# Kernel optimization log

Hardware: AMD Instinct MI355X
Metric: run time of the kernel (lower is better)

Reference implementation:

```python
import jax, jax.numpy as jnp
import numpy as np

FEAT_DOWNSAMPLE = 16  # stage-0 features are 1/16 of input resolution
LOCAL_MAX_DISPS = (12, 3, 3)


def _warp_horizontal(feat, flow):
    # dense_image_warp specialized to 1-channel (horizontal) flow:
    # out[n,y,x,c] = bilinear(feat)[n, y, x - flow[n,y,x,0], c], edge-clamped.
    N, H, W, C = feat.shape
    xq = jnp.arange(W, dtype=feat.dtype)[None, None, :] - flow[..., 0]  # (N,H,W)
    xq = jnp.clip(xq, 0.0, W - 1)
    x0 = jnp.clip(jnp.floor(xq), 0, W - 2).astype(jnp.int32)
    alpha = (xq - x0.astype(feat.dtype))[..., None]  # (N,H,W,1)
    idx0 = jnp.broadcast_to(x0[..., None], (N, H, W, C))
    f0 = jnp.take_along_axis(feat, idx0, axis=2)
    f1 = jnp.take_along_axis(feat, idx0 + 1, axis=2)
    return f0 * (1.0 - alpha) + f1 * alpha


def _build_volume_2d(fl, fr, maxdisp, stride=1):
    # cost[b,h,w,d] = sum_c |fl[b,h,w,c] - fr[b,h,w-d,c]|  (fr treated as 0 for w<d)
    W = fl.shape[2]
    costs = []
    for i in range(0, maxdisp, stride):
        fr_s = fr if i == 0 else jnp.pad(fr, ((0, 0), (0, 0), (i, 0), (0, 0)))[:, :, :W, :]
        costs.append(jnp.sum(jnp.abs(fl - fr_s), axis=-1))
    return jnp.stack(costs, axis=-1)


def _build_volume_2d3(fl, fr, maxdisp, disp, stride=1):
    # Faithful replication of the TF tile+reshape semantics (row-major, same as tf.reshape)
    B, H, W, C = fl.shape
    K = 2 * maxdisp - 1
    bd = jnp.tile(disp[:, :, :, :, None], (1, 1, 1, 1, K)).reshape(-1, H, W, 1)
    shift = jnp.tile(jnp.arange(-maxdisp + 1, maxdisp, dtype=fl.dtype), (B,))[:, None, None, None] * stride
    bd = bd - shift
    bfl = jnp.tile(fl[:, :, :, :, None], (1, 1, 1, 1, K)).reshape(-1, H, W, C)
    bfr = jnp.tile(fr[:, :, :, :, None], (1, 1, 1, 1, K)).reshape(-1, H, W, C)
    norm = jnp.sum(jnp.abs(bfl - _warp_horizontal(bfr, bd)), axis=-1)  # (B*K,H,W)
    return norm.reshape(B, H, W, K)


def _conv3d(x, w):
    return jax.lax.conv_general_dilated(x, w, (1, 1, 1), 'SAME',
                                        dimension_numbers=('NDHWC', 'DHWIO', 'NDHWC'))


def _regularize(x, w_in, w_mid, w_out):
    # Conv3DRegularizer: disp_conv3d_layers ReLU Conv3D(3x3x3) + final 1-channel Conv3D
    x = jax.nn.relu(_conv3d(x, w_in))
    for k in range(w_mid.shape[0]):
        x = jax.nn.relu(_conv3d(x, w_mid[k]))
    return _conv3d(x, w_out)


def _resize(x, h, w):
    return jax.image.resize(x, (x.shape[0], h, w, x.shape[3]), method='bilinear')


def _forward(feats_l0, feats_r0, feats_l1, feats_r1, feats_l2, feats_r2,
             w0_in, w0_mid, w0_out, w1_in, w1_mid, w1_out, w2_in, w2_mid, w2_out):
    feats_l = [feats_l0, feats_l1, feats_l2]
    feats_r = [feats_r0, feats_r1, feats_r2]
    ws = [(w0_in, w0_mid, w0_out), (w1_in, w1_mid, w1_out), (w2_in, w2_mid, w2_out)]
    img_h = feats_l0.shape[1] * FEAT_DOWNSAMPLE
    img_w = feats_l0.shape[2] * FEAT_DOWNSAMPLE
    pred = []
    for scale in range(3):
        fl, fr = feats_l[scale], feats_r[scale]
        md = LOCAL_MAX_DISPS[scale]
        if scale > 0:
            wflow = _resize(pred[scale - 1], fl.shape[1], fl.shape[2]) * (fl.shape[1] / img_h)
            cost = _build_volume_2d3(fl, fr, md, wflow)
        else:
            cost = _build_volume_2d(fl, fr, md)
        cost = _regularize(cost[..., None], *ws[scale])  # (B,H,W,D,1)
        cost = jnp.squeeze(cost, axis=-1)
        sm = jax.nn.softmax(-cost, axis=-1)
        if scale == 0:
            dvals = jnp.arange(0, md, dtype=sm.dtype)
        else:
            dvals = jnp.arange(-md + 1, md, dtype=sm.dtype)
        disp_lr = jnp.sum(sm * dvals[None, None, None, :], axis=-1, keepdims=True)
        disp_up = _resize(disp_lr, img_h, img_w)
        pred.append(disp_up if scale == 0 else disp_up + pred[scale - 1])
    return jnp.stack(pred, axis=0)  # (3, B, imgH, imgW, 1)


def setup_inputs() -> dict:
    key = jax.random.key(0)
    ks = jax.random.split(key, 16)
    B, C = 16, 16
    d = {
        'feats_l0': jax.random.normal(ks[0], (B, 32, 64, C), jnp.float32),
        'feats_r0': jax.random.normal(ks[1], (B, 32, 64, C), jnp.float32),
        'feats_l1': jax.random.normal(ks[2], (B, 64, 128, C), jnp.float32),
        'feats_r1': jax.random.normal(ks[3], (B, 64, 128, C), jnp.float32),
        'feats_l2': jax.random.normal(ks[4], (B, 128, 256, C), jnp.float32),
        'feats_r2': jax.random.normal(ks[5], (B, 128, 256, C), jnp.float32),
        'w0_in': jax.random.normal(ks[6], (3, 3, 3, 1, 16), jnp.float32) * 0.1,
        'w0_mid': jax.random.normal(ks[7], (3, 3, 3, 3, 16, 16), jnp.float32) * 0.1,
        'w0_out': jax.random.normal(ks[8], (3, 3, 3, 16, 1), jnp.float32) * 0.1,
        'w1_in': jax.random.normal(ks[9], (3, 3, 3, 1, 4), jnp.float32) * 0.1,
        'w1_mid': jax.random.normal(ks[10], (3, 3, 3, 3, 4, 4), jnp.float32) * 0.1,
        'w1_out': jax.random.normal(ks[11], (3, 3, 3, 4, 1), jnp.float32) * 0.1,
        'w2_in': jax.random.normal(ks[12], (3, 3, 3, 1, 4), jnp.float32) * 0.1,
        'w2_mid': jax.random.normal(ks[13], (3, 3, 3, 3, 4, 4), jnp.float32) * 0.1,
        'w2_out': jax.random.normal(ks[14], (3, 3, 3, 4, 1), jnp.float32) * 0.1,
    }
    return d


def reference(feats_l0, feats_r0, feats_l1, feats_r1, feats_l2, feats_r2,
              w0_in, w0_mid, w0_out, w1_in, w1_mid, w1_out, w2_in, w2_mid, w2_out):
    return _forward(feats_l0, feats_r0, feats_l1, feats_r1, feats_l2, feats_r2,
                    w0_in, w0_mid, w0_out, w1_in, w1_mid, w1_out, w2_in, w2_mid, w2_out)
```

## Files before the change

### kernel.cpp

```cpp
#include <hip/hip_runtime.h>

#define TPB 256

static inline int cdiv(int a, int b) { return (a + b - 1) / b; }

template <int C>
__global__ void cost0_kernel(const float* __restrict__ fl, const float* __restrict__ fr,
                             float* __restrict__ out, int B, int H, int W, int D) {
    int idx = blockIdx.x * blockDim.x + threadIdx.x;
    int total = B * H * W * D;
    if (idx >= total) return;
    int d = idx % D; int t = idx / D;
    int w = t % W;   t /= W;
    int h = t % H;   int b = t / H;
    const float* pl = fl + (size_t)((b * H + h) * W + w) * C;
    float s = 0.f;
    if (w >= d) {
        const float* pr = fr + (size_t)((b * H + h) * W + (w - d)) * C;
#pragma unroll
        for (int c = 0; c < C; ++c) s += fabsf(pl[c] - pr[c]);
    } else {
#pragma unroll
        for (int c = 0; c < C; ++c) s += fabsf(pl[c]);
    }
    out[idx] = s;
}

template <int C, int K, int W>
__global__ void cost2d3_kernel(const float* __restrict__ fl, const float* __restrict__ fr,
                               const float* __restrict__ wflow, float* __restrict__ out,
                               int B, int H, int md) {
    int idx = blockIdx.x * blockDim.x + threadIdx.x;
    int total = B * K * H * W;
    if (idx >= total) return;
    int x = idx % W; int t0 = idx / W;
    int y = t0 % H;  int n = t0 / H;
    int a = n / K, t = n % K;

    int rem2 = (t * H + y) * W + x;
    int hd = rem2 / (W * K);
    int wd = (rem2 / K) % W;
    float bd = wflow[(a * H + hd) * W + wd] - (float)(t - md + 1);

    float xq = (float)x - bd;
    xq = fminf(fmaxf(xq, 0.f), (float)(W - 1));
    int x0 = (int)floorf(xq);
    if (x0 > W - 2) x0 = W - 2;
    float al = xq - (float)x0;

    int base  = ((t * H + y) * W + x)  * C;
    int base0 = ((t * H + y) * W + x0) * C;
    int base1 = base0 + C;

    float s = 0.f;
#pragma unroll
    for (int c = 0; c < C; ++c) {
        int r = base + c;
        int h1 = r / (W * C * K); int w1 = (r / (C * K)) % W; int c1 = (r / K) % C;
        float av = fl[((a * H + h1) * W + w1) * C + c1];

        int r0 = base0 + c;
        int h0 = r0 / (W * C * K); int w0 = (r0 / (C * K)) % W; int c0 = (r0 / K) % C;
        float f0 = fr[((a * H + h0) * W + w0) * C + c0];

        int r1 = base1 + c;
        int h1b = r1 / (W * C * K); int w1b = (r1 / (C * K)) % W; int c1b = (r1 / K) % C;
        float f1 = fr[((a * H + h1b) * W + w1b) * C + c1b];

        float wv = f0 * (1.f - al) + f1 * al;
        s += fabsf(av - wv);
    }
    out[idx] = s;
}

template <int CIN, int COUT, bool RELU>
__global__ void conv3d_kernel(const float* __restrict__ in, const float* __restrict__ wsrc,
                              float* __restrict__ out, int B, int D1, int D2, int D3) {
    constexpr int WSZ = 27 * CIN * COUT;
    __shared__ float ws[WSZ];
    for (int i = threadIdx.x; i < WSZ; i += blockDim.x) ws[i] = wsrc[i];
    __syncthreads();

    int idx = blockIdx.x * blockDim.x + threadIdx.x;
    int total = B * D1 * D2 * D3;
    if (idx >= total) return;
    int d3 = idx % D3; int t = idx / D3;
    int d2 = t % D2;   t /= D2;
    int d1 = t % D1;   int b = t / D1;

    float acc[COUT];
#pragma unroll
    for (int co = 0; co < COUT; ++co) acc[co] = 0.f;

    for (int kd = 0; kd < 3; ++kd) {
        int z = d1 + kd - 1; if (z < 0 || z >= D1) continue;
        for (int kh = 0; kh < 3; ++kh) {
            int y = d2 + kh - 1; if (y < 0 || y >= D2) continue;
            int rowbase = ((b * D1 + z) * D2 + y) * D3;
            for (int kw = 0; kw < 3; ++kw) {
                int x = d3 + kw - 1; if (x < 0 || x >= D3) continue;
                const float* ip = in + (size_t)(rowbase + x) * CIN;
                const float* wp = ws + ((kd * 3 + kh) * 3 + kw) * CIN * COUT;
#pragma unroll
                for (int ci = 0; ci < CIN; ++ci) {
                    float v = ip[ci];
                    if constexpr (COUT % 4 == 0) {
                        const float4* w4 = (const float4*)(wp + ci * COUT);
#pragma unroll
                        for (int q = 0; q < COUT / 4; ++q) {
                            float4 wv = w4[q];
                            acc[q * 4 + 0] += v * wv.x;
                            acc[q * 4 + 1] += v * wv.y;
                            acc[q * 4 + 2] += v * wv.z;
                            acc[q * 4 + 3] += v * wv.w;
                        }
                    } else {
#pragma unroll
                        for (int co = 0; co < COUT; ++co) acc[co] += v * wp[ci * COUT + co];
                    }
                }
            }
        }
    }

    float* op = out + (size_t)idx * COUT;
#pragma unroll
    for (int co = 0; co < COUT; ++co) op[co] = RELU ? fmaxf(acc[co], 0.f) : acc[co];
}

__global__ void softargmax_kernel(const float* __restrict__ in, float* __restrict__ out,
                                  int npix, int D, float dstart) {
    int idx = blockIdx.x * blockDim.x + threadIdx.x;
    if (idx >= npix) return;
    const float* p = in + (size_t)idx * D;
    float m = -1e30f;
    for (int d = 0; d < D; ++d) m = fmaxf(m, -p[d]);
    float s = 0.f, wsum = 0.f;
    for (int d = 0; d < D; ++d) {
        float e = expf(-p[d] - m);
        s += e;
        wsum += e * (dstart + (float)d);
    }
    out[idx] = wsum / s;
}

__global__ void upsample_kernel(const float* __restrict__ disp, int inH, int inW,
                                const float* __restrict__ prev, float* __restrict__ out,
                                int B, int OH, int OW) {
    int idx = blockIdx.x * blockDim.x + threadIdx.x;
    int total = B * OH * OW;
    if (idx >= total) return;
    int x = idx % OW; int t = idx / OW;
    int y = t % OH;   int b = t / OH;
    float sy = (y + 0.5f) * ((float)inH / (float)OH) - 0.5f;
    float sx = (x + 0.5f) * ((float)inW / (float)OW) - 0.5f;
    sy = fminf(fmaxf(sy, 0.f), (float)(inH - 1));
    sx = fminf(fmaxf(sx, 0.f), (float)(inW - 1));
    int y0 = (int)sy; if (y0 > inH - 2) y0 = inH - 2;
    int x0 = (int)sx; if (x0 > inW - 2) x0 = inW - 2;
    float ay = sy - (float)y0, ax = sx - (float)x0;
    const float* p = disp + (size_t)(b * inH + y0) * inW + x0;
    float v00 = p[0], v01 = p[1], v10 = p[inW], v11 = p[inW + 1];
    float v0 = v00 * (1.f - ax) + v01 * ax;
    float v1 = v10 * (1.f - ax) + v11 * ax;
    float v  = v0 * (1.f - ay) + v1 * ay;
    if (prev) v += prev[idx];
    out[idx] = v;
}

__global__ void downsample_kernel(const float* __restrict__ in, int inH, int inW,
                                  float* __restrict__ out, int B, int OH, int OW,
                                  int F, float mult) {
    int idx = blockIdx.x * blockDim.x + threadIdx.x;
    int total = B * OH * OW;
    if (idx >= total) return;
    int x = idx % OW; int t = idx / OW;
    int y = t % OH;   int b = t / OH;
    float sy = (y + 0.5f) * (float)F - 0.5f;
    float sx = (x + 0.5f) * (float)F - 0.5f;
    float invF = 1.f / (float)F;
    int jlo = (int)floorf(sy) - F + 1, jhi = (int)floorf(sy) + F;
    int ilo = (int)floorf(sx) - F + 1, ihi = (int)floorf(sx) + F;

    float wxsum = 0.f;
    for (int i = ilo; i <= ihi; ++i) {
        if (i < 0 || i >= inW) continue;
        float wx = 1.f - fabsf(sx - (float)i) * invF;
        if (wx > 0.f) wxsum += wx;
    }
    float wysum = 0.f, acc = 0.f;
    for (int j = jlo; j <= jhi; ++j) {
        if (j < 0 || j >= inH) continue;
        float wy = 1.f - fabsf(sy - (float)j) * invF;
        if (wy <= 0.f) continue;
        wysum += wy;
        const float* row = in + (size_t)(b * inH + j) * inW;
        float r = 0.f;
        for (int i = ilo; i <= ihi; ++i) {
            if (i < 0 || i >= inW) continue;
            float wx = 1.f - fabsf(sx - (float)i) * invF;
            if (wx > 0.f) r += wx * row[i];
        }
        acc += wy * r;
    }
    out[idx] = mult * acc / (wysum * wxsum);
}


extern "C" void kernel_launch(void* const* d_in, const int* in_sizes, int n_in,
                              void* d_out, int out_size, void* d_ws, size_t ws_size,
                              hipStream_t stream) {
    const float* fl0 = (const float*)d_in[0];
    const float* fr0 = (const float*)d_in[1];
    const float* fl1 = (const float*)d_in[2];
    const float* fr1 = (const float*)d_in[3];
    const float* fl2 = (const float*)d_in[4];
    const float* fr2 = (const float*)d_in[5];
    const float* w0_in  = (const float*)d_in[6];
    const float* w0_mid = (const float*)d_in[7];
    const float* w0_out = (const float*)d_in[8];
    const float* w1_in  = (const float*)d_in[9];
    const float* w1_mid = (const float*)d_in[10];
    const float* w1_out = (const float*)d_in[11];
    const float* w2_in  = (const float*)d_in[12];
    const float* w2_mid = (const float*)d_in[13];
    const float* w2_out = (const float*)d_in[14];
    float* out = (float*)d_out;

    const int B = 16;
    const int OH = 512, OW = 1024;
    const int P = B * OH * OW;

    const size_t BUF = 10485760;
    float* bufA  = (float*)d_ws;
    float* bufB  = bufA + BUF;
    float* disp  = bufB + BUF;
    float* wflow = disp + 524288;

    {
        const int H = 32, W = 64, D = 12;
        int vox = B * H * W * D;
        cost0_kernel<16><<<cdiv(vox, TPB), TPB, 0, stream>>>(fl0, fr0, bufA, B, H, W, D);
        conv3d_kernel<1, 16, true ><<<cdiv(vox, TPB), TPB, 0, stream>>>(bufA, w0_in,           bufB, B, H, W, D);
        conv3d_kernel<16, 16, true><<<cdiv(vox, TPB), TPB, 0, stream>>>(bufB, w0_mid,          bufA, B, H, W, D);
        conv3d_kernel<16, 16, true><<<cdiv(vox, TPB), TPB, 0, stream>>>(bufA, w0_mid + 6912,   bufB, B, H, W, D);
        conv3d_kernel<16, 16, true><<<cdiv(vox, TPB), TPB, 0, stream>>>(bufB, w0_mid + 13824,  bufA, B, H, W, D);
        conv3d_kernel<16, 1, false><<<cdiv(vox, TPB), TPB, 0, stream>>>(bufA, w0_out,          bufB, B, H, W, D);
        softargmax_kernel<<<cdiv(B * H * W, TPB), TPB, 0, stream>>>(bufB, disp, B * H * W, D, 0.f);
        upsample_kernel<<<cdiv(P, TPB), TPB, 0, stream>>>(disp, H, W, nullptr, out, B, OH, OW);
    }

    {
        const int H = 64, W = 128, K = 5, md = 3;
        downsample_kernel<<<cdiv(B * H * W, TPB), TPB, 0, stream>>>(out, OH, OW, wflow, B, H, W, 8, 64.f / 512.f);
        int vox = B * K * H * W;
        cost2d3_kernel<16, 5, 128><<<cdiv(vox, TPB), TPB, 0, stream>>>(fl1, fr1, wflow, bufA, B, H, md);
        conv3d_kernel<1, 4, true ><<<cdiv(vox, TPB), TPB, 0, stream>>>(bufA, w1_in,        bufB, B, H, W, K);
        conv3d_kernel<4, 4, true ><<<cdiv(vox, TPB), TPB, 0, stream>>>(bufB, w1_mid,       bufA, B, H, W, K);
        conv3d_kernel<4, 4, true ><<<cdiv(vox, TPB), TPB, 0, stream>>>(bufA, w1_mid + 432, bufB, B, H, W, K);
        conv3d_kernel<4, 4, true ><<<cdiv(vox, TPB), TPB, 0, stream>>>(bufB, w1_mid + 864, bufA, B, H, W, K);
        conv3d_kernel<4, 1, false><<<cdiv(vox, TPB), TPB, 0, stream>>>(bufA, w1_out,       bufB, B, H, W, K);
        softargmax_kernel<<<cdiv(B * H * W, TPB), TPB, 0, stream>>>(bufB, disp, B * H * W, K, -2.f);
        upsample_kernel<<<cdiv(P, TPB), TPB, 0, stream>>>(disp, H, W, out, out + P, B, OH, OW);
    }

    {
        const int H = 128, W = 256, K = 5, md = 3;
        downsample_kernel<<<cdiv(B * H * W, TPB), TPB, 0, stream>>>(out + P, OH, OW, wflow, B, H, W, 4, 128.f / 512.f);
        int vox = B * K * H * W;
        cost2d3_kernel<16, 5, 256><<<cdiv(vox, TPB), TPB, 0, stream>>>(fl2, fr2, wflow, bufA, B, H, md);
        conv3d_kernel<1, 4, true ><<<cdiv(vox, TPB), TPB, 0, stream>>>(bufA, w2_in,        bufB, B, H, W, K);
        conv3d_kernel<4, 4, true ><<<cdiv(vox, TPB), TPB, 0, stream>>>(bufB, w2_mid,       bufA, B, H, W, K);
        conv3d_kernel<4, 4, true ><<<cdiv(vox, TPB), TPB, 0, stream>>>(bufA, w2_mid + 432, bufB, B, H, W, K);
        conv3d_kernel<4, 4, true ><<<cdiv(vox, TPB), TPB, 0, stream>>>(bufB, w2_mid + 864, bufA, B, H, W, K);
        conv3d_kernel<4, 1, false><<<cdiv(vox, TPB), TPB, 0, stream>>>(bufA, w2_out,       bufB, B, H, W, K);
        softargmax_kernel<<<cdiv(B * H * W, TPB), TPB, 0, stream>>>(bufB, disp, B * H * W, K, -2.f);
        upsample_kernel<<<cdiv(P, TPB), TPB, 0, stream>>>(disp, H, W, out + P, out + 2 * P, B, OH, OW);
    }
}
```

Baseline: 1.016 ms.

## Register-block conv3d along disparity axis with sliding input window

Replaces the per-voxel conv3d kernel with one where each thread computes T consecutive outputs along the innermost (disparity) axis. A sliding window of T+2 input columns is loaded once per row, with float4 loads when the channel count allows, and reused across the three kw taps. Weights are now read straight from global memory (uniform, cached) instead of being staged in shared memory. This cuts redundant input loads and per-thread index math, at the cost of more registers per thread and fewer threads.

Result: slower. 1.806 ms (+77.8%).

```diff
diff --git a/kernel.cpp b/kernel.cpp
--- a/kernel.cpp
+++ b/kernel.cpp
@@ -73,59 +73,89 @@
     out[idx] = s;
 }
 
-template <int CIN, int COUT, bool RELU>
-__global__ void conv3d_kernel(const float* __restrict__ in, const float* __restrict__ wsrc,
-                              float* __restrict__ out, int B, int D1, int D2, int D3) {
-    constexpr int WSZ = 27 * CIN * COUT;
-    __shared__ float ws[WSZ];
-    for (int i = threadIdx.x; i < WSZ; i += blockDim.x) ws[i] = wsrc[i];
-    __syncthreads();
-
-    int idx = blockIdx.x * blockDim.x + threadIdx.x;
-    int total = B * D1 * D2 * D3;
-    if (idx >= total) return;
-    int d3 = idx % D3; int t = idx / D3;
-    int d2 = t % D2;   t /= D2;
-    int d1 = t % D1;   int b = t / D1;
-
-    float acc[COUT];
-#pragma unroll
-    for (int co = 0; co < COUT; ++co) acc[co] = 0.f;
+template <int CIN, int COUT, int T, bool RELU>
+__global__ void conv3d_blk(const float* __restrict__ in, const float* __restrict__ w,
+                           float* __restrict__ out, int B, int D1, int D2, int D3) {
+    const int nblk = D3 / T;
+    int idx = blockIdx.x * blockDim.x + threadIdx.x;
+    int total = B * D1 * D2 * nblk;
+    if (idx >= total) return;
+    int t3 = (idx % nblk) * T; int t = idx / nblk;
+    int d2 = t % D2; t /= D2;
+    int d1 = t % D1; int b = t / D1;
+
+    float acc[T][COUT];
+#pragma unroll
+    for (int o = 0; o < T; ++o)
+#pragma unroll
+        for (int co = 0; co < COUT; ++co) acc[o][co] = 0.f;
 
     for (int kd = 0; kd < 3; ++kd) {
         int z = d1 + kd - 1; if (z < 0 || z >= D1) continue;
         for (int kh = 0; kh < 3; ++kh) {
             int y = d2 + kh - 1; if (y < 0 || y >= D2) continue;
-            int rowbase = ((b * D1 + z) * D2 + y) * D3;
-            for (int kw = 0; kw < 3; ++kw) {
-                int x = d3 + kw - 1; if (x < 0 || x >= D3) continue;
-                const float* ip = in + (size_t)(rowbase + x) * CIN;
-                const float* wp = ws + ((kd * 3 + kh) * 3 + kw) * CIN * COUT;
+            const float* rowp = in + (size_t)((b * D1 + z) * D2 + y) * D3 * CIN;
+            const float* wbase = w + (kd * 3 + kh) * 3 * CIN * COUT;
+
+            if constexpr (CIN % 4 == 0) {
+#pragma unroll
+                for (int c4 = 0; c4 < CIN / 4; ++c4) {
+                    float seg[(T + 2) * 4];
+#pragma unroll
+                    for (int p = 0; p < T + 2; ++p) {
+                        int x = t3 + p - 1;
+                        float4 v;
+                        if (x >= 0 && x < D3) v = *(const float4*)(rowp + x * CIN + c4 * 4);
+                        else                  v = make_float4(0.f, 0.f, 0.f, 0.f);
+                        seg[p * 4 + 0] = v.x; seg[p * 4 + 1] = v.y;
+                        seg[p * 4 + 2] = v.z; seg[p * 4 + 3] = v.w;
+                    }
+#pragma unroll
+                    for (int kw = 0; kw < 3; ++kw) {
+#pragma unroll
+                        for (int j = 0; j < 4; ++j) {
+                            const float* wp = wbase + (kw * CIN + c4 * 4 + j) * COUT;
+#pragma unroll
+                            for (int co = 0; co < COUT; ++co) {
+                                float wv = wp[co];
+#pragma unroll
+                                for (int o = 0; o < T; ++o)
+                                    acc[o][co] += seg[(o + kw) * 4 + j] * wv;
+                            }
+                        }
+                    }
+                }
+            } else {
 #pragma unroll
                 for (int ci = 0; ci < CIN; ++ci) {
-                    float v = ip[ci];
-                    if constexpr (COUT % 4 == 0) {
-                        const float4* w4 = (const float4*)(wp + ci * COUT);
-#pragma unroll
-                        for (int q = 0; q < COUT / 4; ++q) {
-                            float4 wv = w4[q];
-                            acc[q * 4 + 0] += v * wv.x;
-                            acc[q * 4 + 1] += v * wv.y;
-                            acc[q * 4 + 2] += v * wv.z;
-                            acc[q * 4 + 3] += v * wv.w;
+                    float seg[T + 2];
+#pragma unroll
+                    for (int p = 0; p < T + 2; ++p) {
+                        int x = t3 + p - 1;
+                        seg[p] = (x >= 0 && x < D3) ? rowp[x * CIN + ci] : 0.f;
+                    }
+#pragma unroll
+                    for (int kw = 0; kw < 3; ++kw) {
+                        const float* wp = wbase + (kw * CIN + ci) * COUT;
+#pragma unroll
+                        for (int co = 0; co < COUT; ++co) {
+                            float wv = wp[co];
+#pragma unroll
+                            for (int o = 0; o < T; ++o)
+                                acc[o][co] += seg[o + kw] * wv;
                         }
-                    } else {
-#pragma unroll
-                        for (int co = 0; co < COUT; ++co) acc[co] += v * wp[ci * COUT + co];
                     }
                 }
             }
         }
     }
 
-    float* op = out + (size_t)idx * COUT;
-#pragma unroll
-    for (int co = 0; co < COUT; ++co) op[co] = RELU ? fmaxf(acc[co], 0.f) : acc[co];
+    float* op = out + ((size_t)((b * D1 + d1) * D2 + d2) * D3 + t3) * COUT;
+#pragma unroll
+    for (int o = 0; o < T; ++o)
+#pragma unroll
+        for (int co = 0; co < COUT; ++co)
+            op[o * COUT + co] = RELU ? fmaxf(acc[o][co], 0.f) : acc[o][co];
 }
 
 __global__ void softargmax_kernel(const float* __restrict__ in, float* __restrict__ out,
@@ -240,12 +270,13 @@
     {
         const int H = 32, W = 64, D = 12;
         int vox = B * H * W * D;
+        int thr2 = B * H * W * (D / 2);
         cost0_kernel<16><<<cdiv(vox, TPB), TPB, 0, stream>>>(fl0, fr0, bufA, B, H, W, D);
-        conv3d_kernel<1, 16, true ><<<cdiv(vox, TPB), TPB, 0, stream>>>(bufA, w0_in,           bufB, B, H, W, D);
-        conv3d_kernel<16, 16, true><<<cdiv(vox, TPB), TPB, 0, stream>>>(bufB, w0_mid,          bufA, B, H, W, D);
-        conv3d_kernel<16, 16, true><<<cdiv(vox, TPB), TPB, 0, stream>>>(bufA, w0_mid + 6912,   bufB, B, H, W, D);
-        conv3d_kernel<16, 16, true><<<cdiv(vox, TPB), TPB, 0, stream>>>(bufB, w0_mid + 13824,  bufA, B, H, W, D);
-        conv3d_kernel<16, 1, false><<<cdiv(vox, TPB), TPB, 0, stream>>>(bufA, w0_out,          bufB, B, H, W, D);
+        conv3d_blk<1, 16, 2, true ><<<cdiv(thr2, TPB), TPB, 0, stream>>>(bufA, w0_in,          bufB, B, H, W, D);
+        conv3d_blk<16, 16, 2, true><<<cdiv(thr2, TPB), TPB, 0, stream>>>(bufB, w0_mid,         bufA, B, H, W, D);
+        conv3d_blk<16, 16, 2, true><<<cdiv(thr2, TPB), TPB, 0, stream>>>(bufA, w0_mid + 6912,  bufB, B, H, W, D);
+        conv3d_blk<16, 16, 2, true><<<cdiv(thr2, TPB), TPB, 0, stream>>>(bufB, w0_mid + 13824, bufA, B, H, W, D);
+        conv3d_blk<16, 1, 2, false><<<cdiv(thr2, TPB), TPB, 0, stream>>>(bufA, w0_out,         bufB, B, H, W, D);
         softargmax_kernel<<<cdiv(B * H * W, TPB), TPB, 0, stream>>>(bufB, disp, B * H * W, D, 0.f);
         upsample_kernel<<<cdiv(P, TPB), TPB, 0, stream>>>(disp, H, W, nullptr, out, B, OH, OW);
     }
@@ -254,12 +285,13 @@
         const int H = 64, W = 128, K = 5, md = 3;
         downsample_kernel<<<cdiv(B * H * W, TPB), TPB, 0, stream>>>(out, OH, OW, wflow, B, H, W, 8, 64.f / 512.f);
         int vox = B * K * H * W;
+        int thr5 = B * H * W;
         cost2d3_kernel<16, 5, 128><<<cdiv(vox, TPB), TPB, 0, stream>>>(fl1, fr1, wflow, bufA, B, H, md);
-        conv3d_kernel<1, 4, true ><<<cdiv(vox, TPB), TPB, 0, stream>>>(bufA, w1_in,        bufB, B, H, W, K);
-        conv3d_kernel<4, 4, true ><<<cdiv(vox, TPB), TPB, 0, stream>>>(bufB, w1_mid,       bufA, B, H, W, K);
-        conv3d_kernel<4, 4, true ><<<cdiv(vox, TPB), TPB, 0, stream>>>(bufA, w1_mid + 432, bufB, B, H, W, K);
-        conv3d_kernel<4, 4, true ><<<cdiv(vox, TPB), TPB, 0, stream>>>(bufB, w1_mid + 864, bufA, B, H, W, K);
-        conv3d_kernel<4, 1, false><<<cdiv(vox, TPB), TPB, 0, stream>>>(bufA, w1_out,       bufB, B, H, W, K);
+        conv3d_blk<1, 4, 5, true ><<<cdiv(thr5, TPB), TPB, 0, stream>>>(bufA, w1_in,        bufB, B, H, W, K);
+        conv3d_blk<4, 4, 5, true ><<<cdiv(thr5, TPB), TPB, 0, stream>>>(bufB, w1_mid,       bufA, B, H, W, K);
+        conv3d_blk<4, 4, 5, true ><<<cdiv(thr5, TPB), TPB, 0, stream>>>(bufA, w1_mid + 432, bufB, B, H, W, K);
+        conv3d_blk<4, 4, 5, true ><<<cdiv(thr5, TPB), TPB, 0, stream>>>(bufB, w1_mid + 864, bufA, B, H, W, K);
+        conv3d_blk<4, 1, 5, false><<<cdiv(thr5, TPB), TPB, 0, stream>>>(bufA, w1_out,       bufB, B, H, W, K);
         softargmax_kernel<<<cdiv(B * H * W, TPB), TPB, 0, stream>>>(bufB, disp, B * H * W, K, -2.f);
         upsample_kernel<<<cdiv(P, TPB), TPB, 0, stream>>>(disp, H, W, out, out + P, B, OH, OW);
     }
@@ -268,12 +300,13 @@
         const int H = 128, W = 256, K = 5, md = 3;
         downsample_kernel<<<cdiv(B * H * W, TPB), TPB, 0, stream>>>(out + P, OH, OW, wflow, B, H, W, 4, 128.f / 512.f);
         int vox = B * K * H * W;
+        int thr5 = B * H * W;
         cost2d3_kernel<16, 5, 256><<<cdiv(vox, TPB), TPB, 0, stream>>>(fl2, fr2, wflow, bufA, B, H, md);
-        conv3d_kernel<1, 4, true ><<<cdiv(vox, TPB), TPB, 0, stream>>>(bufA, w2_in,        bufB, B, H, W, K);
-        conv3d_kernel<4, 4, true ><<<cdiv(vox, TPB), TPB, 0, stream>>>(bufB, w2_mid,       bufA, B, H, W, K);
-        conv3d_kernel<4, 4, true ><<<cdiv(vox, TPB), TPB, 0, stream>>>(bufA, w2_mid + 432, bufB, B, H, W, K);
-        conv3d_kernel<4, 4, true ><<<cdiv(vox, TPB), TPB, 0, stream>>>(bufB, w2_mid + 864, bufA, B, H, W, K);
-        conv3d_kernel<4, 1, false><<<cdiv(vox, TPB), TPB, 0, stream>>>(bufA, w2_out,       bufB, B, H, W, K);
+        conv3d_blk<1, 4, 5, true ><<<cdiv(thr5, TPB), TPB, 0, stream>>>(bufA, w2_in,        bufB, B, H, W, K);
+        conv3d_blk<4, 4, 5, true ><<<cdiv(thr5, TPB), TPB, 0, stream>>>(bufB, w2_mid,       bufA, B, H, W, K);
+        conv3d_blk<4, 4, 5, true ><<<cdiv(thr5, TPB), TPB, 0, stream>>>(bufA, w2_mid + 432, bufB, B, H, W, K);
+        conv3d_blk<4, 4, 5, true ><<<cdiv(thr5, TPB), TPB, 0, stream>>>(bufB, w2_mid + 864, bufA, B, H, W, K);
+        conv3d_blk<4, 1, 5, false><<<cdiv(thr5, TPB), TPB, 0, stream>>>(bufA, w2_out,       bufB, B, H, W, K);
         softargmax_kernel<<<cdiv(B * H * W, TPB), TPB, 0, stream>>>(bufB, disp, B * H * W, K, -2.f);
         upsample_kernel<<<cdiv(P, TPB), TPB, 0, stream>>>(disp, H, W, out + P, out + 2 * P, B, OH, OW);
     }
```
